# Performance work log

Measured on AMD Instinct MI355X. Metric: run time of the kernel, lower is better.

## Reference

```python
import jax, jax.numpy as jnp
import numpy as np

B, S, D, K = 8, 4096, 512, 4096
COMMIT = 0.25


def setup_inputs() -> dict:
    key = jax.random.key(0)
    k1, k2, k3, k4 = jax.random.split(key, 4)
    inputs = jax.random.normal(k1, (B, S, D), dtype=jnp.float32)
    # codebook initialized uniform(-1/K, 1/K) as in the torch module
    codebook = jax.random.uniform(k2, (K, D), dtype=jnp.float32, minval=-1.0 / K, maxval=1.0 / K)
    gate_w = jax.random.normal(k3, (D, D), dtype=jnp.float32) * (1.0 / np.sqrt(D))
    gate_b = jax.random.normal(k4, (D,), dtype=jnp.float32) * 0.01
    return {"inputs": inputs, "codebook": codebook, "gate_w": gate_w, "gate_b": gate_b}


def reference(inputs, codebook, gate_w, gate_b):
    d = inputs.shape[-1]
    flat = inputs.reshape(-1, d)  # [N, D]
    # squared L2 distances to all codes: [N, K]
    distances = (jnp.sum(flat * flat, axis=1, keepdims=True)
                 + jnp.sum(codebook * codebook, axis=1)
                 - 2.0 * jnp.matmul(flat, codebook.T))
    idx = jnp.argmin(distances, axis=1)  # [N]
    # one-hot matmul in the original == direct gather
    quantized = jnp.take(codebook, idx, axis=0).reshape(inputs.shape)
    e_latent_loss = jnp.mean((jax.lax.stop_gradient(quantized) - inputs) ** 2)
    q_latent_loss = jnp.mean((quantized - jax.lax.stop_gradient(inputs)) ** 2)
    loss = q_latent_loss + COMMIT * e_latent_loss
    # straight-through estimator
    quantized_st = inputs + jax.lax.stop_gradient(quantized - inputs)
    gate = jax.nn.sigmoid(jnp.matmul(inputs, gate_w.T) + gate_b)
    output = inputs + quantized_st * gate
    return output, loss
```

## Files before the change

### kernel.cpp

```cpp
#include <hip/hip_runtime.h>
#include <hip/hip_bf16.h>

typedef unsigned short u16;
typedef unsigned char u8;
typedef float f32x4 __attribute__((ext_vector_type(4)));
typedef int i32x4 __attribute__((ext_vector_type(4)));

#define NTOK 32768
#define DIM  512
#define KC   4096

__device__ __forceinline__ void gload_lds16(const void* g, void* l) {
  __builtin_amdgcn_global_load_lds(
      (__attribute__((address_space(1))) void*)g,
      (__attribute__((address_space(3))) void*)l,
      16, 0, 0);
}

__device__ __forceinline__ unsigned pk4(float a, float b, float c, float d, float inv) {
  int b0 = __float2int_rn(a * inv), b1 = __float2int_rn(b * inv);
  int b2 = __float2int_rn(c * inv), b3 = __float2int_rn(d * inv);
  return (unsigned)(b0 & 255) | ((unsigned)(b1 & 255) << 8) |
         ((unsigned)(b2 & 255) << 16) | ((unsigned)(b3 & 255) << 24);
}

__device__ __forceinline__ size_t swz_dst(int row, int lane) {
  int chunk = lane >> 3;
  int s8    = lane & 7;
  int h     = (row >> 1) & 3;
  return (size_t)row * DIM + chunk * 64 + ((((s8 >> 1) ^ h) << 4) | ((s8 & 1) << 3));
}

__global__ void cvt_x_i8(const float* __restrict__ in, u8* __restrict__ q,
                         float* __restrict__ xs) {
  int row  = blockIdx.x * 4 + (threadIdx.x >> 6);
  int lane = threadIdx.x & 63;
  const float* src = in + (size_t)row * DIM + lane * 8;
  float4 a = *reinterpret_cast<const float4*>(src);
  float4 b = *reinterpret_cast<const float4*>(src + 4);
  float m = fmaxf(fmaxf(fmaxf(fabsf(a.x), fabsf(a.y)), fmaxf(fabsf(a.z), fabsf(a.w))),
                  fmaxf(fmaxf(fabsf(b.x), fabsf(b.y)), fmaxf(fabsf(b.z), fabsf(b.w))));
#pragma unroll
  for (int s = 1; s < 64; s <<= 1) m = fmaxf(m, __shfl_xor(m, s, 64));
  float inv = 127.0f / fmaxf(m, 1e-20f);
  uint2 w2;
  w2.x = pk4(a.x, a.y, a.z, a.w, inv);
  w2.y = pk4(b.x, b.y, b.z, b.w, inv);
  *reinterpret_cast<uint2*>(q + swz_dst(row, lane)) = w2;
  if (lane == 0) xs[row] = m * (1.0f / 127.0f);
}

__global__ void cvt_cb_i8(const float* __restrict__ cb, u8* __restrict__ cq,
                          float* __restrict__ cnorm, float* __restrict__ cs2) {
  int row  = blockIdx.x * 4 + (threadIdx.x >> 6);
  int lane = threadIdx.x & 63;
  const float* src = cb + (size_t)row * DIM + lane * 8;
  float4 a = *reinterpret_cast<const float4*>(src);
  float4 b = *reinterpret_cast<const float4*>(src + 4);
  float m = fmaxf(fmaxf(fmaxf(fabsf(a.x), fabsf(a.y)), fmaxf(fabsf(a.z), fabsf(a.w))),
                  fmaxf(fmaxf(fabsf(b.x), fabsf(b.y)), fmaxf(fabsf(b.z), fabsf(b.w))));
  float s = a.x*a.x + a.y*a.y + a.z*a.z + a.w*a.w
          + b.x*b.x + b.y*b.y + b.z*b.z + b.w*b.w;
#pragma unroll
  for (int sh = 1; sh < 64; sh <<= 1) {
    m = fmaxf(m, __shfl_xor(m, sh, 64));
    s += __shfl_xor(s, sh, 64);
  }
  float inv = 127.0f / fmaxf(m, 1e-20f);
  uint2 w2;
  w2.x = pk4(a.x, a.y, a.z, a.w, inv);
  w2.y = pk4(b.x, b.y, b.z, b.w, inv);
  *reinterpret_cast<uint2*>(cq + swz_dst(row, lane)) = w2;
  if (lane == 0) { cnorm[row] = s; cs2[row] = 2.0f * m * (1.0f / 127.0f); }
}

__global__ void cvt_w_i8(const float* __restrict__ w, u8* __restrict__ wq,
                         float* __restrict__ ws) {
  int row  = blockIdx.x * 4 + (threadIdx.x >> 6);
  int lane = threadIdx.x & 63;
  const float* src = w + (size_t)row * DIM + lane * 8;
  float4 a = *reinterpret_cast<const float4*>(src);
  float4 b = *reinterpret_cast<const float4*>(src + 4);
  float m = fmaxf(fmaxf(fmaxf(fabsf(a.x), fabsf(a.y)), fmaxf(fabsf(a.z), fabsf(a.w))),
                  fmaxf(fmaxf(fabsf(b.x), fabsf(b.y)), fmaxf(fabsf(b.z), fabsf(b.w))));
#pragma unroll
  for (int s = 1; s < 64; s <<= 1) m = fmaxf(m, __shfl_xor(m, s, 64));
  float inv = 127.0f / fmaxf(m, 1e-20f);
  uint2 w2;
  w2.x = pk4(a.x, a.y, a.z, a.w, inv);
  w2.y = pk4(b.x, b.y, b.z, b.w, inv);
  *reinterpret_cast<uint2*>(wq + swz_dst(row, lane)) = w2;
  if (lane == 0) ws[row] = m * (1.0f / 127.0f);
}

__global__ __launch_bounds__(256)
void argmin_i8(const u8* __restrict__ Xq, const u8* __restrict__ Cq,
               const float* __restrict__ cnorm, const float* __restrict__ cs2,
               const float* __restrict__ xs,
               float* __restrict__ pval, int* __restrict__ pidx) {
  __shared__ __align__(16) u8 As[2][128 * 64];
  __shared__ __align__(16) u8 Bs[2][128 * 64];

  const int tid  = threadIdx.x;
  const int lane = tid & 63;
  const int wid  = tid >> 6;
  const int wr   = wid >> 1;
  const int wc   = wid & 1;
  const int bm   = blockIdx.x;
  const int bn   = blockIdx.y;
  const int l15  = lane & 15, l4 = lane >> 4;

  const u8* Xg = Xq + (size_t)(bm * 128) * DIM;
  const u8* Cg = Cq + (size_t)(bn * 128) * DIM;

  auto stage = [&](int buf, int kt) {
    int kk = kt * 64;
#pragma unroll
    for (int p = 0; p < 2; p++) {
      int row = p * 64 + wid * 16 + (lane >> 2);
      gload_lds16(Xg + (size_t)row * DIM + kk + (lane & 3) * 16,
                  (void*)(As[buf] + (p * 64 + wid * 16) * 64));
      gload_lds16(Cg + (size_t)row * DIM + kk + (lane & 3) * 16,
                  (void*)(Bs[buf] + (p * 64 + wid * 16) * 64));
    }
  };

  auto rd16 = [&](const u8* base, int row) -> i32x4 {
    return *reinterpret_cast<const i32x4*>(
        base + row * 64 + ((l4 ^ ((row >> 1) & 3)) << 4));
  };

  i32x4 acc[4][4];
#pragma unroll
  for (int i = 0; i < 4; i++)
#pragma unroll
    for (int j = 0; j < 4; j++)
#pragma unroll
      for (int r = 0; r < 4; r++) acc[i][j][r] = 0;

  stage(0, 0);
  stage(1, 1);
  asm volatile("s_waitcnt vmcnt(4)" ::: "memory");
  __builtin_amdgcn_s_barrier();
  asm volatile("" ::: "memory");

  for (int t = 0; t < 8; ++t) {
    const u8* Xt = As[t & 1];
    const u8* Ct = Bs[t & 1];
    i32x4 xfr[4];
#pragma unroll
    for (int ni = 0; ni < 4; ni++) xfr[ni] = rd16(Xt, wc * 64 + ni * 16 + l15);
#pragma unroll
    for (int mi = 0; mi < 4; mi++) {
      i32x4 cf = rd16(Ct, wr * 64 + mi * 16 + l15);
      __builtin_amdgcn_s_setprio(1);
#pragma unroll
      for (int ni = 0; ni < 4; ni++)
        acc[mi][ni] = __builtin_amdgcn_mfma_i32_16x16x64_i8(
            cf, xfr[ni], acc[mi][ni], 0, 0, 0);
      __builtin_amdgcn_s_setprio(0);
    }

    asm volatile("" ::: "memory");
    __builtin_amdgcn_s_barrier();
    asm volatile("" ::: "memory");
    if (t + 2 < 8) {
      stage(t & 1, t + 2);
      asm volatile("s_waitcnt vmcnt(4)" ::: "memory");
      __builtin_amdgcn_s_barrier();
      asm volatile("" ::: "memory");
    } else if (t < 7) {
      asm volatile("s_waitcnt vmcnt(0)" ::: "memory");
      __builtin_amdgcn_s_barrier();
      asm volatile("" ::: "memory");
    }
  }

  float cn[4][4], c2q[4][4];
#pragma unroll
  for (int mi = 0; mi < 4; mi++)
#pragma unroll
    for (int r = 0; r < 4; r++) {
      int code = bn * 128 + wr * 64 + mi * 16 + l4 * 4 + r;
      cn[mi][r]  = cnorm[code];
      c2q[mi][r] = cs2[code];
    }

  float* rv = (float*)As;
  int*   ri = (int*)Bs;
  __syncthreads();

#pragma unroll
  for (int ni = 0; ni < 4; ni++) {
    int token = bm * 128 + wc * 64 + ni * 16 + l15;
    float xsv = xs[token];
    float best = 1e30f;
    int bi = 0;
#pragma unroll
    for (int mi = 0; mi < 4; mi++)
#pragma unroll
      for (int r = 0; r < 4; r++) {
        float v = fmaf(-xsv * c2q[mi][r], (float)acc[mi][ni][r], cn[mi][r]);
        int code = bn * 128 + wr * 64 + mi * 16 + l4 * 4 + r;
        if (v < best) { best = v; bi = code; }
      }
#pragma unroll
    for (int m = 16; m < 64; m <<= 1) {
      float ov = __shfl_xor(best, m, 64);
      int   oi = __shfl_xor(bi, m, 64);
      if (ov < best) { best = ov; bi = oi; }
    }
    if (l4 == 0) {
      int tl = wc * 64 + ni * 16 + l15;
      rv[wr * 128 + tl] = best;
      ri[wr * 128 + tl] = bi;
    }
  }
  __syncthreads();
  if (tid < 128) {
    float bv = rv[tid];
    int   bb = ri[tid];
    float v1 = rv[128 + tid];
    if (v1 < bv) { bv = v1; bb = ri[128 + tid]; }
    size_t g = (size_t)bn * NTOK + bm * 128 + tid;
    pval[g] = bv;
    pidx[g] = bb;
  }
}

__global__ void argmin_reduce(const float* __restrict__ pval, const int* __restrict__ pidx,
                              int* __restrict__ idx) {
  int t = blockIdx.x * 256 + threadIdx.x;
  float best = 1e30f;
  int bi = 0;
  for (int c = 0; c < 32; c++) {
    float v = pval[(size_t)c * NTOK + t];
    if (v < best) { best = v; bi = pidx[(size_t)c * NTOK + t]; }
  }
  idx[t] = bi;
}

__global__ __launch_bounds__(512, 4)
void gate_i8(const u8* __restrict__ Xq, const u8* __restrict__ Wq,
             const float* __restrict__ X, const float* __restrict__ Cf,
             const float* __restrict__ gb, const float* __restrict__ xs,
             const float* __restrict__ ws, const int* __restrict__ idx,
             float* __restrict__ out, float* __restrict__ blockSum) {
  __shared__ __align__(16) u8 As[2][128 * 64];
  __shared__ __align__(16) u8 Bs[2][256 * 64];
  __shared__ float bsum[8];

  const int tid  = threadIdx.x;
  const int lane = tid & 63;
  const int wid  = tid >> 6;
  const int wr   = wid >> 2;
  const int wc   = wid & 3;
  const int bm   = blockIdx.x;
  const int bn   = blockIdx.y;
  const int l15  = lane & 15, l4 = lane >> 4;

  const u8* Xg = Xq + (size_t)(bm * 128) * DIM;
  const u8* Wg = Wq + (size_t)(bn * 256) * DIM;

  auto stage = [&](int buf, int kt) {
    int kk = kt * 64;
    {
      int row = wid * 16 + (lane >> 2);
      gload_lds16(Xg + (size_t)row * DIM + kk + (lane & 3) * 16,
                  (void*)(As[buf] + wid * 1024));
    }
#pragma unroll
    for (int p = 0; p < 2; p++) {
      int row = p * 128 + wid * 16 + (lane >> 2);
      gload_lds16(Wg + (size_t)row * DIM + kk + (lane & 3) * 16,
                  (void*)(Bs[buf] + p * 8192 + wid * 1024));
    }
  };

  auto rd16 = [&](const u8* base, int row) -> i32x4 {
    return *reinterpret_cast<const i32x4*>(
        base + row * 64 + ((l4 ^ ((row >> 1) & 3)) << 4));
  };

  i32x4 acc[4][4];
#pragma unroll
  for (int i = 0; i < 4; i++)
#pragma unroll
    for (int j = 0; j < 4; j++)
#pragma unroll
      for (int r = 0; r < 4; r++) acc[i][j][r] = 0;

  stage(0, 0);
  stage(1, 1);
  asm volatile("s_waitcnt vmcnt(3)" ::: "memory");
  __builtin_amdgcn_s_barrier();
  asm volatile("" ::: "memory");

  for (int t = 0; t < 8; ++t) {
    const u8* A  = As[t & 1];
    const u8* Bt = Bs[t & 1];
    i32x4 bfr[4];
#pragma unroll
    for (int ni = 0; ni < 4; ni++) bfr[ni] = rd16(Bt, wc * 64 + ni * 16 + l15);
#pragma unroll
    for (int mi = 0; mi < 4; mi++) {
      i32x4 af = rd16(A, wr * 64 + mi * 16 + l15);
      __builtin_amdgcn_s_setprio(1);
#pragma unroll
      for (int ni = 0; ni < 4; ni++)
        acc[mi][ni] = __builtin_amdgcn_mfma_i32_16x16x64_i8(
            af, bfr[ni], acc[mi][ni], 0, 0, 0);
      __builtin_amdgcn_s_setprio(0);
    }

    asm volatile("" ::: "memory");
    __builtin_amdgcn_s_barrier();
    asm volatile("" ::: "memory");
    if (t + 2 < 8) {
      stage(t & 1, t + 2);
      asm volatile("s_waitcnt vmcnt(3)" ::: "memory");
      __builtin_amdgcn_s_barrier();
      asm volatile("" ::: "memory");
    } else if (t < 7) {
      asm volatile("s_waitcnt vmcnt(0)" ::: "memory");
      __builtin_amdgcn_s_barrier();
      asm volatile("" ::: "memory");
    }
  }

  float wsv[4], gbv[4];
  int   cl[4];
#pragma unroll
  for (int ni = 0; ni < 4; ni++) {
    cl[ni] = bn * 256 + wc * 64 + ni * 16 + l15;
    wsv[ni] = ws[cl[ni]];
    gbv[ni] = gb[cl[ni]];
  }
  float lsum = 0.f;
#pragma unroll
  for (int mi = 0; mi < 4; mi++) {
#pragma unroll
    for (int r = 0; r < 4; r++) {
      int token = bm * 128 + wr * 64 + mi * 16 + l4 * 4 + r;
      int code = idx[token];
      float xsv = xs[token];
#pragma unroll
      for (int ni = 0; ni < 4; ni++) {
        int col = cl[ni];
        float logit = xsv * wsv[ni] * (float)acc[mi][ni][r] + gbv[ni];
        float g = 1.0f / (1.0f + __expf(-logit));
        float q = Cf[(size_t)code * DIM + col];
        float xx = X[(size_t)token * DIM + col];
        out[(size_t)token * DIM + col] = xx + q * g;
        float d = q - xx;
        lsum += d * d;
      }
    }
  }
#pragma unroll
  for (int m = 1; m < 64; m <<= 1) lsum += __shfl_xor(lsum, m, 64);
  if (lane == 0) bsum[wid] = lsum;
  __syncthreads();
  if (tid == 0) {
    float s = 0.f;
#pragma unroll
    for (int i = 0; i < 8; i++) s += bsum[i];
    blockSum[blockIdx.y * gridDim.x + blockIdx.x] = s;
  }
}

__global__ void finalize(const float* __restrict__ blockSum, float* __restrict__ out_loss) {
  int t = threadIdx.x;
  float s = blockSum[t * 2] + blockSum[t * 2 + 1];
#pragma unroll
  for (int m = 1; m < 64; m <<= 1) s += __shfl_xor(s, m, 64);
  __shared__ float w4[4];
  if ((t & 63) == 0) w4[t >> 6] = s;
  __syncthreads();
  if (t == 0) {
    float tot = w4[0] + w4[1] + w4[2] + w4[3];
    out_loss[0] = 1.25f * tot / 16777216.0f;
  }
}

extern "C" void kernel_launch(void* const* d_in, const int* in_sizes, int n_in,
                              void* d_out, int out_size, void* d_ws, size_t ws_size,
                              hipStream_t stream) {
  const float* X  = (const float*)d_in[0];
  const float* CB = (const float*)d_in[1];
  const float* GW = (const float*)d_in[2];
  const float* GB = (const float*)d_in[3];
  float* out = (float*)d_out;

  char* w = (char*)d_ws;
  size_t off = 0;
  auto alloc = [&](size_t bytes) -> void* {
    void* p = w + off;
    off = (off + bytes + 255) & ~(size_t)255;
    return p;
  };
  u8*    Xq    = (u8*) alloc((size_t)NTOK * DIM);
  u8*    Cq    = (u8*) alloc((size_t)KC * DIM);
  u8*    Wq    = (u8*) alloc((size_t)DIM * DIM);
  float* xsc   = (float*)alloc((size_t)NTOK * 4);
  float* cnorm = (float*)alloc((size_t)KC * 4);
  float* cs2   = (float*)alloc((size_t)KC * 4);
  float* wsc   = (float*)alloc((size_t)DIM * 4);
  float* pval  = (float*)alloc((size_t)32 * NTOK * 4);
  int*   pidx  = (int*)alloc((size_t)32 * NTOK * 4);
  int*   idx   = (int*)alloc((size_t)NTOK * 4);
  float* bsums = (float*)alloc((size_t)512 * 4);

  cvt_x_i8<<<8192, 256, 0, stream>>>(X, Xq, xsc);
  cvt_cb_i8<<<1024, 256, 0, stream>>>(CB, Cq, cnorm, cs2);
  cvt_w_i8<<<128, 256, 0, stream>>>(GW, Wq, wsc);
  argmin_i8<<<dim3(256, 32), 256, 0, stream>>>(Xq, Cq, cnorm, cs2, xsc, pval, pidx);
  argmin_reduce<<<128, 256, 0, stream>>>(pval, pidx, idx);
  gate_i8<<<dim3(256, 2), 512, 0, stream>>>(Xq, Wq, X, CB, GB, xsc, wsc, idx, out, bsums);
  finalize<<<1, 256, 0, stream>>>(bsums, out + (size_t)NTOK * DIM);
}
```

Baseline: 169.3 us.

## Keep token tile resident in LDS and sweep codebook halves per block

The argmin kernel now loads the full 128-token × 512-dim int8 tile into LDS once. Each block then loops over 16 code groups, covering 2048 codes instead of 128. The running min and index are kept in registers across groups, so the grid shrinks from 32 to 2 code-column blocks and the partial-argmin buffers and reduce kernel handle 2 partials instead of 32. This removes repeated X reloads, most of the partial writes and the reduce reads. In exchange LDS per block grows to about 80KB, which lowers occupancy and leaves fewer blocks to hide latency.

New measurement: 181.5 us. 7.2% more time.

```diff
diff --git a/kernel.cpp b/kernel.cpp
--- a/kernel.cpp
+++ b/kernel.cpp
@@ -98,8 +98,8 @@
                const float* __restrict__ cnorm, const float* __restrict__ cs2,
                const float* __restrict__ xs,
                float* __restrict__ pval, int* __restrict__ pidx) {
-  __shared__ __align__(16) u8 As[2][128 * 64];
-  __shared__ __align__(16) u8 Bs[2][128 * 64];
+  __shared__ __align__(16) u8 Xs[8 * 128 * 64];
+  __shared__ __align__(16) u8 Cs[2][128 * 64];
 
   const int tid  = threadIdx.x;
   const int lane = tid & 63;
@@ -107,29 +107,47 @@
   const int wr   = wid >> 1;
   const int wc   = wid & 1;
   const int bm   = blockIdx.x;
-  const int bn   = blockIdx.y;
+  const int bnH  = blockIdx.y;
   const int l15  = lane & 15, l4 = lane >> 4;
 
   const u8* Xg = Xq + (size_t)(bm * 128) * DIM;
-  const u8* Cg = Cq + (size_t)(bn * 128) * DIM;
-
-  auto stage = [&](int buf, int kt) {
-    int kk = kt * 64;
+  const u8* Cg = Cq + (size_t)(bnH * 2048) * DIM;
+
+  auto stageX = [&]() {
+#pragma unroll
+    for (int t = 0; t < 8; t++)
+#pragma unroll
+      for (int p = 0; p < 2; p++) {
+        int row = p * 64 + wid * 16 + (lane >> 2);
+        gload_lds16(Xg + (size_t)row * DIM + t * 64 + (lane & 3) * 16,
+                    (void*)(Xs + t * 8192 + (p * 64 + wid * 16) * 64));
+      }
+  };
+  auto stageC = [&](int buf, int s) {
+    int g = s >> 3, t = s & 7;
+    const u8* base = Cg + (size_t)(g * 128) * DIM + t * 64;
 #pragma unroll
     for (int p = 0; p < 2; p++) {
       int row = p * 64 + wid * 16 + (lane >> 2);
-      gload_lds16(Xg + (size_t)row * DIM + kk + (lane & 3) * 16,
-                  (void*)(As[buf] + (p * 64 + wid * 16) * 64));
-      gload_lds16(Cg + (size_t)row * DIM + kk + (lane & 3) * 16,
-                  (void*)(Bs[buf] + (p * 64 + wid * 16) * 64));
-    }
-  };
-
+      gload_lds16(base + (size_t)row * DIM + (lane & 3) * 16,
+                  (void*)(Cs[buf] + (p * 64 + wid * 16) * 64));
+    }
+  };
   auto rd16 = [&](const u8* base, int row) -> i32x4 {
     return *reinterpret_cast<const i32x4*>(
         base + row * 64 + ((l4 ^ ((row >> 1) & 3)) << 4));
   };
 
+  float xsv[4];
+  float best[4];
+  int   bi[4];
+#pragma unroll
+  for (int ni = 0; ni < 4; ni++) {
+    xsv[ni]  = xs[bm * 128 + wc * 64 + ni * 16 + l15];
+    best[ni] = 1e30f;
+    bi[ni]   = 0;
+  }
+
   i32x4 acc[4][4];
 #pragma unroll
   for (int i = 0; i < 4; i++)
@@ -138,15 +156,17 @@
 #pragma unroll
       for (int r = 0; r < 4; r++) acc[i][j][r] = 0;
 
-  stage(0, 0);
-  stage(1, 1);
-  asm volatile("s_waitcnt vmcnt(4)" ::: "memory");
+  stageX();
+  stageC(0, 0);
+  stageC(1, 1);
+  asm volatile("s_waitcnt vmcnt(2)" ::: "memory");
   __builtin_amdgcn_s_barrier();
   asm volatile("" ::: "memory");
 
-  for (int t = 0; t < 8; ++t) {
-    const u8* Xt = As[t & 1];
-    const u8* Ct = Bs[t & 1];
+  const int NS = 128;
+  for (int s = 0; s < NS; ++s) {
+    const u8* Ct = Cs[s & 1];
+    const u8* Xt = Xs + (s & 7) * 8192;
     i32x4 xfr[4];
 #pragma unroll
     for (int ni = 0; ni < 4; ni++) xfr[ni] = rd16(Xt, wc * 64 + ni * 16 + l15);
@@ -161,59 +181,67 @@
       __builtin_amdgcn_s_setprio(0);
     }
 
+    if ((s & 7) == 7) {
+      int gbase = bnH * 2048 + (s >> 3) * 128 + wr * 64;
+      float cn[4][4], c2q[4][4];
+#pragma unroll
+      for (int mi = 0; mi < 4; mi++)
+#pragma unroll
+        for (int r = 0; r < 4; r++) {
+          int code = gbase + mi * 16 + l4 * 4 + r;
+          cn[mi][r]  = cnorm[code];
+          c2q[mi][r] = cs2[code];
+        }
+#pragma unroll
+      for (int ni = 0; ni < 4; ni++)
+#pragma unroll
+        for (int mi = 0; mi < 4; mi++)
+#pragma unroll
+          for (int r = 0; r < 4; r++) {
+            float v = fmaf(-xsv[ni] * c2q[mi][r], (float)acc[mi][ni][r], cn[mi][r]);
+            if (v < best[ni]) { best[ni] = v; bi[ni] = gbase + mi * 16 + l4 * 4 + r; }
+          }
+#pragma unroll
+      for (int i = 0; i < 4; i++)
+#pragma unroll
+        for (int j = 0; j < 4; j++)
+#pragma unroll
+          for (int r = 0; r < 4; r++) acc[i][j][r] = 0;
+    }
+
     asm volatile("" ::: "memory");
     __builtin_amdgcn_s_barrier();
     asm volatile("" ::: "memory");
-    if (t + 2 < 8) {
-      stage(t & 1, t + 2);
-      asm volatile("s_waitcnt vmcnt(4)" ::: "memory");
+    if (s + 2 < NS) {
+      stageC(s & 1, s + 2);
+      asm volatile("s_waitcnt vmcnt(2)" ::: "memory");
       __builtin_amdgcn_s_barrier();
       asm volatile("" ::: "memory");
-    } else if (t < 7) {
+    } else if (s == NS - 2) {
       asm volatile("s_waitcnt vmcnt(0)" ::: "memory");
       __builtin_amdgcn_s_barrier();
       asm volatile("" ::: "memory");
     }
   }
 
-  float cn[4][4], c2q[4][4];
-#pragma unroll
-  for (int mi = 0; mi < 4; mi++)
-#pragma unroll
-    for (int r = 0; r < 4; r++) {
-      int code = bn * 128 + wr * 64 + mi * 16 + l4 * 4 + r;
-      cn[mi][r]  = cnorm[code];
-      c2q[mi][r] = cs2[code];
-    }
-
-  float* rv = (float*)As;
-  int*   ri = (int*)Bs;
+  float* rv = (float*)Cs[0];
+  int*   ri = (int*)Cs[1];
   __syncthreads();
 
 #pragma unroll
   for (int ni = 0; ni < 4; ni++) {
-    int token = bm * 128 + wc * 64 + ni * 16 + l15;
-    float xsv = xs[token];
-    float best = 1e30f;
-    int bi = 0;
-#pragma unroll
-    for (int mi = 0; mi < 4; mi++)
-#pragma unroll
-      for (int r = 0; r < 4; r++) {
-        float v = fmaf(-xsv * c2q[mi][r], (float)acc[mi][ni][r], cn[mi][r]);
-        int code = bn * 128 + wr * 64 + mi * 16 + l4 * 4 + r;
-        if (v < best) { best = v; bi = code; }
-      }
+    float b = best[ni];
+    int   c = bi[ni];
 #pragma unroll
     for (int m = 16; m < 64; m <<= 1) {
-      float ov = __shfl_xor(best, m, 64);
-      int   oi = __shfl_xor(bi, m, 64);
-      if (ov < best) { best = ov; bi = oi; }
+      float ov = __shfl_xor(b, m, 64);
+      int   oi = __shfl_xor(c, m, 64);
+      if (ov < b) { b = ov; c = oi; }
     }
     if (l4 == 0) {
       int tl = wc * 64 + ni * 16 + l15;
-      rv[wr * 128 + tl] = best;
-      ri[wr * 128 + tl] = bi;
+      rv[wr * 128 + tl] = b;
+      ri[wr * 128 + tl] = c;
     }
   }
   __syncthreads();
@@ -222,7 +250,7 @@
     int   bb = ri[tid];
     float v1 = rv[128 + tid];
     if (v1 < bv) { bv = v1; bb = ri[128 + tid]; }
-    size_t g = (size_t)bn * NTOK + bm * 128 + tid;
+    size_t g = (size_t)bnH * NTOK + bm * 128 + tid;
     pval[g] = bv;
     pidx[g] = bb;
   }
@@ -231,13 +259,9 @@
 __global__ void argmin_reduce(const float* __restrict__ pval, const int* __restrict__ pidx,
                               int* __restrict__ idx) {
   int t = blockIdx.x * 256 + threadIdx.x;
-  float best = 1e30f;
-  int bi = 0;
-  for (int c = 0; c < 32; c++) {
-    float v = pval[(size_t)c * NTOK + t];
-    if (v < best) { best = v; bi = pidx[(size_t)c * NTOK + t]; }
-  }
-  idx[t] = bi;
+  float v0 = pval[t], v1 = pval[(size_t)NTOK + t];
+  int   i0 = pidx[t], i1 = pidx[(size_t)NTOK + t];
+  idx[t] = (v1 < v0) ? i1 : i0;
 }
 
 __global__ __launch_bounds__(512, 4)
@@ -406,15 +430,15 @@
   float* cnorm = (float*)alloc((size_t)KC * 4);
   float* cs2   = (float*)alloc((size_t)KC * 4);
   float* wsc   = (float*)alloc((size_t)DIM * 4);
-  float* pval  = (float*)alloc((size_t)32 * NTOK * 4);
-  int*   pidx  = (int*)alloc((size_t)32 * NTOK * 4);
+  float* pval  = (float*)alloc((size_t)2 * NTOK * 4);
+  int*   pidx  = (int*)alloc((size_t)2 * NTOK * 4);
   int*   idx   = (int*)alloc((size_t)NTOK * 4);
   float* bsums = (float*)alloc((size_t)512 * 4);
 
   cvt_x_i8<<<8192, 256, 0, stream>>>(X, Xq, xsc);
   cvt_cb_i8<<<1024, 256, 0, stream>>>(CB, Cq, cnorm, cs2);
   cvt_w_i8<<<128, 256, 0, stream>>>(GW, Wq, wsc);
-  argmin_i8<<<dim3(256, 32), 256, 0, stream>>>(Xq, Cq, cnorm, cs2, xsc, pval, pidx);
+  argmin_i8<<<dim3(256, 2), 256, 0, stream>>>(Xq, Cq, cnorm, cs2, xsc, pval, pidx);
   argmin_reduce<<<128, 256, 0, stream>>>(pval, pidx, idx);
   gate_i8<<<dim3(256, 2), 512, 0, stream>>>(Xq, Wq, X, CB, GB, xsc, wsc, idx, out, bsums);
   finalize<<<1, 256, 0, stream>>>(bsums, out + (size_t)NTOK * DIM);
```
